# Performance work log

Hardware: AMD Instinct MI355X
Metric: run time of the kernel (lower is better)

The kernel has to match this reference:

```python
import jax, jax.numpy as jnp
import numpy as np

NUM_ENT_CLASS = 150
NORMED_REL_VEC_DIST = False


def box_cxcywh_to_xyxy(b):
    cx, cy, w, h = b[..., 0], b[..., 1], b[..., 2], b[..., 3]
    return jnp.stack([cx - 0.5 * w, cy - 0.5 * h, cx + 0.5 * w, cy + 0.5 * h], axis=-1)


def box_xyxy_to_cxcywh(b):
    x0, y0, x1, y1 = b[..., 0], b[..., 1], b[..., 2], b[..., 3]
    return jnp.stack([(x0 + x1) * 0.5, (y0 + y1) * 0.5, x1 - x0, y1 - y0], axis=-1)


def generalized_box_iou(a, b):
    # a: [N,4], b: [M,4], xyxy -> [N,M]
    area_a = (a[:, 2] - a[:, 0]) * (a[:, 3] - a[:, 1])
    area_b = (b[:, 2] - b[:, 0]) * (b[:, 3] - b[:, 1])
    lt = jnp.maximum(a[:, None, :2], b[None, :, :2])
    rb = jnp.minimum(a[:, None, 2:], b[None, :, 2:])
    wh = jnp.clip(rb - lt, 0.0)
    inter = wh[..., 0] * wh[..., 1]
    union = area_a[:, None] + area_b[None, :] - inter
    iou = inter / union
    lt_c = jnp.minimum(a[:, None, :2], b[None, :, :2])
    rb_c = jnp.maximum(a[:, None, 2:], b[None, :, 2:])
    wh_c = jnp.clip(rb_c - lt_c, 0.0)
    area_c = wh_c[..., 0] * wh_c[..., 1]
    return iou - (area_c - union) / area_c


def cdist_l2(a, b):
    # a: [N,C], b: [M,C] -> [N,M] euclidean distance (gram-matrix form)
    d2 = (jnp.sum(a * a, -1)[:, None] + jnp.sum(b * b, -1)[None, :]
          - 2.0 * (a @ b.T))
    return jnp.sqrt(jnp.maximum(d2, 1e-12))


def _per_image(ent_box_n, ent_logits, ro_logits, rs_logits, ro_box_n, rs_box_n,
               rel_vec_n, scale):
    # scale: [4] = [w, h, w, h]
    ent_box = box_cxcywh_to_xyxy(ent_box_n) * scale[None, :]           # [Ne,4] pixels
    ent_cnter = box_xyxy_to_cxcywh(ent_box)[..., :2]                    # [Ne,2]
    ent_cnter_normed = ent_box_n[..., :2]

    # num_ent_class (150) != logits dim (151) -> softmax, drop background
    ro_dist = jax.nn.softmax(ro_logits, axis=-1)[..., :-1]              # [Nr,150]
    rs_dist = jax.nn.softmax(rs_logits, axis=-1)[..., :-1]
    ent_prob = jax.nn.softmax(ent_logits, axis=-1)[..., :-1]            # [Ne,150]
    ent_score = jnp.max(ent_prob, axis=-1)                              # [Ne]

    ro_box = box_cxcywh_to_xyxy(ro_box_n) * scale[None, :]              # [Nr,4]
    rs_box = box_cxcywh_to_xyxy(rs_box_n) * scale[None, :]
    rel_vec = rel_vec_n * scale[None, :]                                # [Nr,4]

    if NORMED_REL_VEC_DIST:
        vec, sc, oc = rel_vec_n, ent_cnter_normed, ent_cnter_normed
    else:
        vec, sc, oc = rel_vec, ent_cnter, ent_cnter

    # L1 distance of rel-vector endpoints to entity centers -> [Nr,Ne]
    dist_s = (jnp.abs(vec[:, None, 0] - sc[None, :, 0])
              + jnp.abs(vec[:, None, 1] - sc[None, :, 1]))
    dist_o = (jnp.abs(vec[:, None, 2] - oc[None, :, 0])
              + jnp.abs(vec[:, None, 3] - oc[None, :, 1]))
    match_vec_sub = 1.0 / (dist_s + 1.0)
    match_vec_obj = 1.0 / (dist_o + 1.0)

    m_s = ent_score[None, :] * match_vec_sub                            # conf-weighted
    m_o = ent_score[None, :] * match_vec_obj

    sub_giou = jnp.clip(generalized_box_iou(ent_box, rs_box), 0.0)      # [Ne,Nr]
    obj_giou = jnp.clip(generalized_box_iou(ent_box, ro_box), 0.0)

    sub_cls = 1.0 / (cdist_l2(rs_dist, ent_prob) + 1.0)                 # [Nr,Ne]
    obj_cls = 1.0 / (cdist_l2(ro_dist, ent_prob) + 1.0)

    dist_s_final = m_s * sub_cls * sub_giou.T                           # [Nr,Ne]
    dist_o_final = m_o * obj_cls * obj_giou.T
    return dist_s_final, dist_o_final


def setup_inputs() -> dict:
    key = jax.random.key(0)
    ks = jax.random.split(key, 8)
    B, Ne, Nr, C1 = 64, 500, 500, NUM_ENT_CLASS + 1
    inp = {
        "pred_boxes": jax.random.uniform(ks[0], (B, Ne, 4), jnp.float32),
        "pred_logits": jax.random.normal(ks[1], (B, Ne, C1), jnp.float32),
        "pred_rel_obj_logits": jax.random.normal(ks[2], (B, Nr, C1), jnp.float32),
        "pred_rel_sub_logits": jax.random.normal(ks[3], (B, Nr, C1), jnp.float32),
        "pred_rel_obj_box": jax.random.uniform(ks[4], (B, Nr, 4), jnp.float32),
        "pred_rel_sub_box": jax.random.uniform(ks[5], (B, Nr, 4), jnp.float32),
        "pred_rel_vec": jax.random.uniform(ks[6], (B, Nr, 4), jnp.float32),
        "target_sizes": 600.0 + 600.0 * jax.random.uniform(ks[7], (B, 2), jnp.float32),
    }
    return inp


def reference(pred_boxes, pred_logits, pred_rel_obj_logits, pred_rel_sub_logits,
              pred_rel_obj_box, pred_rel_sub_box, pred_rel_vec, target_sizes):
    img_h, img_w = target_sizes[:, 0], target_sizes[:, 1]
    scale_fct = jnp.stack([img_w, img_h, img_w, img_h], axis=1)  # [B,4]
    sub_dist, obj_dist = jax.vmap(_per_image)(
        pred_boxes, pred_logits, pred_rel_obj_logits, pred_rel_sub_logits,
        pred_rel_obj_box, pred_rel_sub_box, pred_rel_vec, scale_fct)
    return sub_dist, obj_dist
```

## Files before the change

kernel.cpp:

```cpp
#include <hip/hip_runtime.h>
#include <math.h>

#define NB   64
#define NPT  500
#define C1   151
#define CM1  150
#define EAF  12
#define RAF  20

#define GRP_ELEMS  2560
#define IMG_ELEMS  (32 * GRP_ELEMS)
#define PROB_ELEMS ((size_t)NB * IMG_ELEMS)

typedef __bf16 bf16x8 __attribute__((ext_vector_type(8)));
typedef float  f32x4  __attribute__((ext_vector_type(4)));

__device__ __forceinline__ float rcpf(float x) { return __builtin_amdgcn_rcpf(x); }
__device__ __forceinline__ float rsqf(float x) { return __builtin_amdgcn_rsqf(x); }

extern "C" __global__ void __launch_bounds__(256)
k_pre(const float* __restrict__ boxes, const float* __restrict__ ent_logits,
      const float* __restrict__ ro_logits, const float* __restrict__ rs_logits,
      const float* __restrict__ ro_box, const float* __restrict__ rs_box,
      const float* __restrict__ rel_vec, const float* __restrict__ tsz,
      __bf16* __restrict__ entP, __bf16* __restrict__ rsP, __bf16* __restrict__ roP,
      float* __restrict__ entAux, float* __restrict__ relAux)
{
    __shared__ __align__(16) __bf16 sP[GRP_ELEMS];

    const int tid = threadIdx.x;
    const int q   = tid & 15;
    const int rl  = tid >> 4;
    const int bx  = blockIdx.x;
    const int set = bx >> 11;
    const int rem = bx & 2047;
    const int b   = rem >> 5;
    const int g   = rem & 31;
    const int i   = g * 16 + rl;
    const bool valid = (i < NPT);
    const int rowIdx = b * NPT + i;

    const float* src = (set == 0 ? ent_logits : (set == 1 ? rs_logits : ro_logits))
                       + (size_t)rowIdx * C1;

    float x[10];
    if (valid) {
        #pragma unroll
        for (int t = 0; t < 9; ++t) x[t] = src[q + 16 * t];
        x[9] = (q <= 6) ? src[q + 144] : -INFINITY;
    } else {
        #pragma unroll
        for (int t = 0; t < 9; ++t) x[t] = 0.f;
        x[9] = -INFINITY;
    }

    float mAll = x[0];
    #pragma unroll
    for (int t = 1; t < 10; ++t) mAll = fmaxf(mAll, x[t]);
    float mKept = x[0];
    #pragma unroll
    for (int t = 1; t < 9; ++t) mKept = fmaxf(mKept, x[t]);
    if (q <= 5) mKept = fmaxf(mKept, x[9]);

    #pragma unroll
    for (int off = 1; off < 16; off <<= 1) {
        mAll  = fmaxf(mAll,  __shfl_xor(mAll,  off, 16));
        mKept = fmaxf(mKept, __shfl_xor(mKept, off, 16));
    }

    float e[10], s = 0.f, s2 = 0.f;
    #pragma unroll
    for (int t = 0; t < 9; ++t) {
        e[t] = __expf(x[t] - mAll);
        s  += e[t];
        s2 += e[t] * e[t];
    }
    e[9] = (q <= 6) ? __expf(x[9] - mAll) : 0.f;
    s += e[9];
    if (q <= 5) s2 += e[9] * e[9];

    #pragma unroll
    for (int off = 1; off < 16; off <<= 1) {
        s  += __shfl_xor(s,  off, 16);
        s2 += __shfl_xor(s2, off, 16);
    }

    const float inv = rcpf(s);
    const float pm  = __expf(mKept - mAll) * inv;
    const float nn  = s2 * inv * inv;

    const int base = rl * 8 + (q & 7);
    const int qh   = q >> 3;
    #pragma unroll
    for (int t = 0; t < 9; ++t)
        sP[(2 * t + qh) * 128 + base] = valid ? (__bf16)(e[t] * inv) : (__bf16)0.f;
    sP[(18 + qh) * 128 + base] = (valid && q <= 5) ? (__bf16)(e[9] * inv) : (__bf16)0.f;

    if (q == 0 && valid) {
        const float hh = tsz[b * 2 + 0];
        const float ww = tsz[b * 2 + 1];
        if (set == 0) {
            const float* bb = boxes + (size_t)rowIdx * 4;
            const float cx = bb[0], cy = bb[1], bw = bb[2], bh = bb[3];
            const float X0 = (cx - 0.5f * bw) * ww, Y0 = (cy - 0.5f * bh) * hh;
            const float X1 = (cx + 0.5f * bw) * ww, Y1 = (cy + 0.5f * bh) * hh;
            float* A = entAux + (size_t)rowIdx * EAF;
            A[0] = pm;
            A[1] = 0.5f * (X0 + X1);
            A[2] = 0.5f * (Y0 + Y1);
            A[3] = nn;
            A[4] = X0; A[5] = Y0; A[6] = X1; A[7] = Y1;
            A[8] = (X1 - X0) * (Y1 - Y0);
            A[9] = X1 - X0;
            A[10] = Y1 - Y0;
        } else if (set == 1) {
            const float* bb = rs_box  + (size_t)rowIdx * 4;
            const float* vv = rel_vec + (size_t)rowIdx * 4;
            const float cx = bb[0], cy = bb[1], bw = bb[2], bh = bb[3];
            float* A = relAux + (size_t)rowIdx * RAF;
            const float X0 = (cx - 0.5f * bw) * ww, Y0 = (cy - 0.5f * bh) * hh;
            const float X1 = (cx + 0.5f * bw) * ww, Y1 = (cy + 0.5f * bh) * hh;
            A[0] = X0; A[1] = Y0; A[2] = X1; A[3] = Y1;
            A[8]  = vv[0] * ww; A[9]  = vv[1] * hh;
            A[10] = vv[2] * ww; A[11] = vv[3] * hh;
            A[12] = nn;
            A[14] = (X1 - X0) * (Y1 - Y0);
            A[16] = X1 - X0;
            A[17] = Y1 - Y0;
        } else {
            const float* bb = ro_box + (size_t)rowIdx * 4;
            const float cx = bb[0], cy = bb[1], bw = bb[2], bh = bb[3];
            float* A = relAux + (size_t)rowIdx * RAF;
            const float X0 = (cx - 0.5f * bw) * ww, Y0 = (cy - 0.5f * bh) * hh;
            const float X1 = (cx + 0.5f * bw) * ww, Y1 = (cy + 0.5f * bh) * hh;
            A[4] = X0; A[5] = Y0; A[6] = X1; A[7] = Y1;
            A[13] = nn;
            A[15] = (X1 - X0) * (Y1 - Y0);
            A[18] = X1 - X0;
            A[19] = Y1 - Y0;
        }
    }

    __syncthreads();

    __bf16* dstT = (set == 0 ? entP : (set == 1 ? rsP : roP));
    float4* dstG = (float4*)(dstT + ((size_t)b * 32 + g) * GRP_ELEMS);
    const float4* srcL = (const float4*)sP;
    dstG[tid] = srcL[tid];
    if (tid < 64) dstG[256 + tid] = srcL[256 + tid];
}

template <bool FULL>
__device__ __forceinline__ void epilogue(
    const float (*eA)[EAF], const float (*rA)[RAF],
    const f32x4* accS, const f32x4* accO,
    int lr, int kq, int wv, int b, int e0T, int r0T,
    float* __restrict__ outS, float* __restrict__ outO)
{
    f32x4 ev0[4], ev1[4];
    float eAr[4], eW[4], eH[4];
    #pragma unroll
    for (int et = 0; et < 4; ++et) {
        const float* ep = eA[et * 16 + lr];
        ev0[et] = *(const f32x4*)(ep);
        ev1[et] = *(const f32x4*)(ep + 4);
        eAr[et] = ep[8]; eW[et] = ep[9]; eH[et] = ep[10];
    }

    const unsigned baseR0 = ((unsigned)b * NPT + (unsigned)(r0T + wv * 16 + kq * 4)) * NPT;
    const unsigned eBase  = (unsigned)(e0T + lr);

    #pragma unroll
    for (int reg = 0; reg < 4; ++reg) {
        const int rIdx = wv * 16 + kq * 4 + reg;
        const bool rOK = FULL || (r0T + rIdx < NPT);
        const float* rp = rA[rIdx];
        const f32x4 rsB = *(const f32x4*)(rp);
        const f32x4 roB = *(const f32x4*)(rp + 4);
        const f32x4 vv  = *(const f32x4*)(rp + 8);
        const f32x4 rn  = *(const f32x4*)(rp + 12);
        const f32x4 rw  = *(const f32x4*)(rp + 16);
        const unsigned rowOff = baseR0 + (unsigned)reg * NPT;

        #pragma unroll
        for (int et = 0; et < 4; ++et) {
            const float score = ev0[et][0], ecx = ev0[et][1], ecy = ev0[et][2], en2 = ev0[et][3];
            const float ex0 = ev1[et][0], ey0 = ev1[et][1], ex1 = ev1[et][2], ey1 = ev1[et][3];
            const float aE = eAr[et];

            const float iwrS = fminf(ex1, rsB[2]) - fmaxf(ex0, rsB[0]);
            const float ihrS = fminf(ey1, rsB[3]) - fmaxf(ey0, rsB[1]);
            const float inS  = fmaxf(iwrS, 0.f) * fmaxf(ihrS, 0.f);
            const float aCS  = ((eW[et] + rw[0]) - iwrS) * ((eH[et] + rw[1]) - ihrS);
            const float unS  = (aE + rn[2]) - inS;
            const float uaS  = unS * aCS;
            const float numS = fmaxf(score * (fmaf(inS, aCS, unS * unS) - uaS), 0.f);
            const float d2s  = fmaxf(fmaf(-2.f, accS[et][reg], rn[0] + en2), 1e-12f);
            const float dS   = d2s * rsqf(d2s);
            const float distS= fabsf(vv[0] - ecx) + fabsf(vv[1] - ecy);
            const float vS   = numS * rcpf(uaS * (distS + 1.f) * (dS + 1.f));

            const float iwrO = fminf(ex1, roB[2]) - fmaxf(ex0, roB[0]);
            const float ihrO = fminf(ey1, roB[3]) - fmaxf(ey0, roB[1]);
            const float inO  = fmaxf(iwrO, 0.f) * fmaxf(ihrO, 0.f);
            const float aCO  = ((eW[et] + rw[2]) - iwrO) * ((eH[et] + rw[3]) - ihrO);
            const float unO  = (aE + rn[3]) - inO;
            const float uaO  = unO * aCO;
            const float numO = fmaxf(score * (fmaf(inO, aCO, unO * unO) - uaO), 0.f);
            const float d2o  = fmaxf(fmaf(-2.f, accO[et][reg], rn[1] + en2), 1e-12f);
            const float dO   = d2o * rsqf(d2o);
            const float distO= fabsf(vv[2] - ecx) + fabsf(vv[3] - ecy);
            const float vO   = numO * rcpf(uaO * (distO + 1.f) * (dO + 1.f));

            const unsigned o = rowOff + eBase + (unsigned)(et * 16);
            if (FULL || (rOK && (int)(eBase + et * 16) < NPT)) {
                outS[o] = vS;
                outO[o] = vO;
            }
        }
    }
}

extern "C" __global__ void __launch_bounds__(256, 4)
k_main(const __bf16* __restrict__ entP, const __bf16* __restrict__ rsP,
       const __bf16* __restrict__ roP, const float* __restrict__ eAuxG,
       const float* __restrict__ rAuxG,
       float* __restrict__ outS, float* __restrict__ outO)
{
    __shared__ __align__(16) __bf16 sEnt[4 * GRP_ELEMS];
    __shared__ __align__(16) float eA[64][EAF];
    __shared__ __align__(16) float rA[64][RAF];

    const int tid = threadIdx.x;
    const int b   = blockIdx.x;
    const int e0T = (blockIdx.y & 7) * 64;
    const int r0T = (blockIdx.y >> 3) * 64;

    const int wv   = tid >> 6;
    const int lane = tid & 63;
    const int lr   = lane & 15;
    const int kq   = lane >> 4;

    const int gR = (r0T >> 4) + wv;
    const int gE = (e0T >> 4);
    const __bf16* rsBase = rsP  + ((size_t)b * 32 + gR) * GRP_ELEMS + lr * 8;
    const __bf16* roBase = roP  + ((size_t)b * 32 + gR) * GRP_ELEMS + lr * 8;
    const __bf16* entSrc = entP + ((size_t)b * 32 + gE) * GRP_ELEMS;

    bf16x8 ars[5], aro[5];
    #pragma unroll
    for (int ks = 0; ks < 5; ++ks) {
        const int kOff = (ks * 4 + kq) * 128;
        ars[ks] = *(const bf16x8*)(rsBase + kOff);
        aro[ks] = *(const bf16x8*)(roBase + kOff);
    }

    #pragma unroll
    for (int it = 0; it < 5; ++it) {
        const int off = it * 4096 + wv * 1024;
        __builtin_amdgcn_global_load_lds(
            (const __attribute__((address_space(1))) unsigned int*)
                ((const char*)entSrc + off + lane * 16),
            (__attribute__((address_space(3))) unsigned int*)
                ((char*)sEnt + off),
            16, 0, 0);
    }

    {
        const float4 z = {0.f, 0.f, 0.f, 0.f};
        for (int t = tid; t < 64 * (EAF / 4); t += 256) {
            const int e = t / (EAF / 4), qq = t % (EAF / 4);
            const int ge = e0T + e;
            ((float4*)eA[e])[qq] = (ge < NPT)
                ? ((const float4*)(eAuxG + ((size_t)b * NPT + ge) * EAF))[qq] : z;
        }
        for (int t = tid; t < 64 * (RAF / 4); t += 256) {
            const int r = t / (RAF / 4), qq = t % (RAF / 4);
            const int gr = r0T + r;
            ((float4*)rA[r])[qq] = (gr < NPT)
                ? ((const float4*)(rAuxG + ((size_t)b * NPT + gr) * RAF))[qq] : z;
        }
    }
    __syncthreads();

    f32x4 accS[4] = {{0,0,0,0},{0,0,0,0},{0,0,0,0},{0,0,0,0}};
    f32x4 accO[4] = {{0,0,0,0},{0,0,0,0},{0,0,0,0},{0,0,0,0}};

    #pragma unroll
    for (int ks = 0; ks < 5; ++ks) {
        const int kOff = (ks * 4 + kq) * 128 + lr * 8;
        #pragma unroll
        for (int et = 0; et < 4; ++et) {
            const bf16x8 be = *(const bf16x8*)&sEnt[et * GRP_ELEMS + kOff];
            accS[et] = __builtin_amdgcn_mfma_f32_16x16x32_bf16(ars[ks], be, accS[et], 0, 0, 0);
            accO[et] = __builtin_amdgcn_mfma_f32_16x16x32_bf16(aro[ks], be, accO[et], 0, 0, 0);
        }
    }

    if (e0T + 64 <= NPT && r0T + 64 <= NPT) {
        epilogue<true >(eA, rA, accS, accO, lr, kq, wv, b, e0T, r0T, outS, outO);
    } else {
        epilogue<false>(eA, rA, accS, accO, lr, kq, wv, b, e0T, r0T, outS, outO);
    }
}

extern "C" void kernel_launch(void* const* d_in, const int* in_sizes, int n_in,
                              void* d_out, int out_size, void* d_ws, size_t ws_size,
                              hipStream_t stream)
{
    const float* boxes      = (const float*)d_in[0];
    const float* ent_logits = (const float*)d_in[1];
    const float* ro_logits  = (const float*)d_in[2];
    const float* rs_logits  = (const float*)d_in[3];
    const float* ro_box     = (const float*)d_in[4];
    const float* rs_box     = (const float*)d_in[5];
    const float* rel_vec    = (const float*)d_in[6];
    const float* tsz        = (const float*)d_in[7];

    __bf16* entP = (__bf16*)d_ws;
    __bf16* rsP  = entP + PROB_ELEMS;
    __bf16* roP  = rsP  + PROB_ELEMS;
    float*  eAux = (float*)(roP + PROB_ELEMS);
    float*  rAux = eAux + (size_t)NB * NPT * EAF;

    float* outS = (float*)d_out;
    float* outO = outS + (size_t)NB * NPT * NPT;

    hipLaunchKernelGGL(k_pre, dim3(6144), dim3(256), 0, stream,
                       boxes, ent_logits, ro_logits, rs_logits,
                       ro_box, rs_box, rel_vec, tsz,
                       entP, rsP, roP, eAux, rAux);

    hipLaunchKernelGGL(k_main, dim3(64, 64), dim3(256), 0, stream,
                       entP, rsP, roP, eAux, rAux, outS, outO);
}
```

Baseline: 231.1 us.

## Widen k_main entity tile to 128 and use nontemporal output stores

Each k_main block now covers 128 entities instead of 64, so the relation A-fragments held in registers are reused across twice as many MFMA tiles and the grid is halved. The epilogue runs twice per block, once per 64-entity half. Output stores become nontemporal to avoid polluting cache with the large write-only result. The trade-off is doubled LDS and accumulator registers, which lowers the occupancy target from 4 to 3 blocks per CU.

```diff
diff --git a/kernel.cpp b/kernel.cpp
--- a/kernel.cpp
+++ b/kernel.cpp
@@ -214,27 +214,27 @@
 
             const unsigned o = rowOff + eBase + (unsigned)(et * 16);
             if (FULL || (rOK && (int)(eBase + et * 16) < NPT)) {
-                outS[o] = vS;
-                outO[o] = vO;
+                __builtin_nontemporal_store(vS, &outS[o]);
+                __builtin_nontemporal_store(vO, &outO[o]);
             }
         }
     }
 }
 
-extern "C" __global__ void __launch_bounds__(256, 4)
+extern "C" __global__ void __launch_bounds__(256, 3)
 k_main(const __bf16* __restrict__ entP, const __bf16* __restrict__ rsP,
        const __bf16* __restrict__ roP, const float* __restrict__ eAuxG,
        const float* __restrict__ rAuxG,
        float* __restrict__ outS, float* __restrict__ outO)
 {
-    __shared__ __align__(16) __bf16 sEnt[4 * GRP_ELEMS];
-    __shared__ __align__(16) float eA[64][EAF];
+    __shared__ __align__(16) __bf16 sEnt[8 * GRP_ELEMS];
+    __shared__ __align__(16) float eA[128][EAF];
     __shared__ __align__(16) float rA[64][RAF];
 
     const int tid = threadIdx.x;
     const int b   = blockIdx.x;
-    const int e0T = (blockIdx.y & 7) * 64;
-    const int r0T = (blockIdx.y >> 3) * 64;
+    const int e0T = (blockIdx.y & 3) * 128;
+    const int r0T = (blockIdx.y >> 2) * 64;
 
     const int wv   = tid >> 6;
     const int lane = tid & 63;
@@ -256,7 +256,7 @@
     }
 
     #pragma unroll
-    for (int it = 0; it < 5; ++it) {
+    for (int it = 0; it < 10; ++it) {
         const int off = it * 4096 + wv * 1024;
         __builtin_amdgcn_global_load_lds(
             (const __attribute__((address_space(1))) unsigned int*)
@@ -268,7 +268,7 @@
 
     {
         const float4 z = {0.f, 0.f, 0.f, 0.f};
-        for (int t = tid; t < 64 * (EAF / 4); t += 256) {
+        for (int t = tid; t < 128 * (EAF / 4); t += 256) {
             const int e = t / (EAF / 4), qq = t % (EAF / 4);
             const int ge = e0T + e;
             ((float4*)eA[e])[qq] = (ge < NPT)
@@ -283,24 +283,35 @@
     }
     __syncthreads();
 
-    f32x4 accS[4] = {{0,0,0,0},{0,0,0,0},{0,0,0,0},{0,0,0,0}};
-    f32x4 accO[4] = {{0,0,0,0},{0,0,0,0},{0,0,0,0},{0,0,0,0}};
+    f32x4 accS0[4] = {{0,0,0,0},{0,0,0,0},{0,0,0,0},{0,0,0,0}};
+    f32x4 accO0[4] = {{0,0,0,0},{0,0,0,0},{0,0,0,0},{0,0,0,0}};
+    f32x4 accS1[4] = {{0,0,0,0},{0,0,0,0},{0,0,0,0},{0,0,0,0}};
+    f32x4 accO1[4] = {{0,0,0,0},{0,0,0,0},{0,0,0,0},{0,0,0,0}};
 
     #pragma unroll
     for (int ks = 0; ks < 5; ++ks) {
         const int kOff = (ks * 4 + kq) * 128 + lr * 8;
         #pragma unroll
         for (int et = 0; et < 4; ++et) {
-            const bf16x8 be = *(const bf16x8*)&sEnt[et * GRP_ELEMS + kOff];
-            accS[et] = __builtin_amdgcn_mfma_f32_16x16x32_bf16(ars[ks], be, accS[et], 0, 0, 0);
-            accO[et] = __builtin_amdgcn_mfma_f32_16x16x32_bf16(aro[ks], be, accO[et], 0, 0, 0);
-        }
-    }
-
-    if (e0T + 64 <= NPT && r0T + 64 <= NPT) {
-        epilogue<true >(eA, rA, accS, accO, lr, kq, wv, b, e0T, r0T, outS, outO);
+            const bf16x8 be0 = *(const bf16x8*)&sEnt[et * GRP_ELEMS + kOff];
+            const bf16x8 be1 = *(const bf16x8*)&sEnt[(4 + et) * GRP_ELEMS + kOff];
+            accS0[et] = __builtin_amdgcn_mfma_f32_16x16x32_bf16(ars[ks], be0, accS0[et], 0, 0, 0);
+            accO0[et] = __builtin_amdgcn_mfma_f32_16x16x32_bf16(aro[ks], be0, accO0[et], 0, 0, 0);
+            accS1[et] = __builtin_amdgcn_mfma_f32_16x16x32_bf16(ars[ks], be1, accS1[et], 0, 0, 0);
+            accO1[et] = __builtin_amdgcn_mfma_f32_16x16x32_bf16(aro[ks], be1, accO1[et], 0, 0, 0);
+        }
+    }
+
+    const bool rFull = (r0T + 64 <= NPT);
+    if (rFull) {
+        epilogue<true >(eA, rA, accS0, accO0, lr, kq, wv, b, e0T, r0T, outS, outO);
     } else {
-        epilogue<false>(eA, rA, accS, accO, lr, kq, wv, b, e0T, r0T, outS, outO);
+        epilogue<false>(eA, rA, accS0, accO0, lr, kq, wv, b, e0T, r0T, outS, outO);
+    }
+    if (rFull && e0T + 128 <= NPT) {
+        epilogue<true >(&eA[64], rA, accS1, accO1, lr, kq, wv, b, e0T + 64, r0T, outS, outO);
+    } else {
+        epilogue<false>(&eA[64], rA, accS1, accO1, lr, kq, wv, b, e0T + 64, r0T, outS, outO);
     }
 }
 
@@ -331,6 +342,6 @@
                        ro_box, rs_box, rel_vec, tsz,
                        entP, rsP, roP, eAux, rAux);
 
-    hipLaunchKernelGGL(k_main, dim3(64, 64), dim3(256), 0, stream,
+    hipLaunchKernelGGL(k_main, dim3(64, 32), dim3(256), 0, stream,
                        entP, rsP, roP, eAux, rAux, outS, outO);
 }
```

Result: slower. 281.0 us (+21.6%).
